# Kernel optimization log

Measured on AMD Instinct MI355X. Metric: run time of the kernel, lower is better.

Reference implementation:

```python
import jax, jax.numpy as jnp
import numpy as np

N, F_IN, F_OUT = 8192, 512, 128
NEG_SLOPE = 0.2
MASK_VAL = -9e16


def setup_inputs() -> dict:
    key = jax.random.key(0)
    k_x, k_adj, k_w, k_a = jax.random.split(key, 4)
    x = jax.random.normal(k_x, (N, F_IN), dtype=jnp.float32)
    adj = jax.random.randint(k_adj, (N, N), 0, 2, dtype=jnp.int32)
    # xavier_normal_ init: std = sqrt(2 / (fan_in + fan_out))
    w = jax.random.normal(k_w, (F_IN, F_OUT), dtype=jnp.float32) * np.sqrt(2.0 / (F_IN + F_OUT))
    a = jax.random.normal(k_a, (2 * F_OUT, 1), dtype=jnp.float32) * np.sqrt(2.0 / (2 * F_OUT + 1))
    return {"x": x, "adj": adj, "w": w, "a": a}


def reference(x, adj, w, a):
    f_out = w.shape[1]
    h = x @ w                                   # [N, f_out]
    source_scores = h @ a[:f_out]               # [N, 1]
    target_scores = h @ a[f_out:]               # [N, 1]
    e = source_scores + target_scores.T         # [N, N] outer sum
    e = jax.nn.leaky_relu(e, negative_slope=NEG_SLOPE)
    e = jnp.where(adj > 0, e, jnp.float32(MASK_VAL))
    attention = jax.nn.softmax(e, axis=-1)      # [N, N]
    h_prime = attention @ h                     # [N, f_out]
    return attention, h_prime
```

## Files before the change

kernel.cpp:

```cpp
#include <hip/hip_runtime.h>
#include <hip/hip_bf16.h>

typedef unsigned short u16;
typedef unsigned int u32;
typedef __attribute__((ext_vector_type(8))) short short8;
typedef __attribute__((ext_vector_type(4))) float f32x4;
typedef __attribute__((ext_vector_type(4))) int i32x4;

#define NN 8192
#define FIN 512
#define FOUT 128
#define NEG 0.2f
#define L2E 1.44269504088896340736f
#define EXP2(x) __builtin_amdgcn_exp2f(x)
#define LOG2(x) __builtin_amdgcn_logf(x)

__device__ __forceinline__ u16 f2bf(float f) {
  u32 u = __builtin_bit_cast(u32, f);
  u32 r = (u + 0x7fffu + ((u >> 16) & 1u)) >> 16;
  return (u16)r;
}

__global__ __launch_bounds__(256) void k_h(const float* __restrict__ x,
                                           const float* __restrict__ w,
                                           const float* __restrict__ av,
                                           u16* __restrict__ hb,
                                           float* __restrict__ sg,
                                           float* __restrict__ tgo) {
  __shared__ float xs[16][68];
  __shared__ float ws_[64][128];
  __shared__ u16 ht[16][130];
  const int t = threadIdx.x;
  const int r0 = blockIdx.x * 16;
  const int r = t >> 4;
  const int cq = (t & 15) * 4;
  float acc[2][4] = {};
  for (int kc = 0; kc < FIN; kc += 64) {
    __syncthreads();
    {
      const int rr = t >> 4, cc = (t & 15) * 4;
      *(float4*)&xs[rr][cc] = *(const float4*)(x + (size_t)(r0 + rr) * FIN + kc + cc);
    }
#pragma unroll
    for (int i = 0; i < 8; ++i) {
      const int off = i * 1024 + t * 4;
      const int wr = off >> 7, wc = off & 127;
      *(float4*)&ws_[wr][wc] = *(const float4*)(w + (size_t)(kc + wr) * FOUT + wc);
    }
    __syncthreads();
    for (int kk = 0; kk < 64; ++kk) {
      const float xv = xs[r][kk];
#pragma unroll
      for (int g = 0; g < 2; ++g) {
        const float4 wv = *(const float4*)&ws_[kk][cq + 64 * g];
        acc[g][0] = fmaf(xv, wv.x, acc[g][0]);
        acc[g][1] = fmaf(xv, wv.y, acc[g][1]);
        acc[g][2] = fmaf(xv, wv.z, acc[g][2]);
        acc[g][3] = fmaf(xv, wv.w, acc[g][3]);
      }
    }
  }
  const int rg = r0 + r;
  float sp = 0.f, tp = 0.f;
#pragma unroll
  for (int g = 0; g < 2; ++g) {
#pragma unroll
    for (int e = 0; e < 4; ++e) {
      const int n = cq + 64 * g + e;
      const float v = acc[g][e];
      ht[r][n] = f2bf(v);
      sp = fmaf(v, av[n], sp);
      tp = fmaf(v, av[FOUT + n], tp);
    }
  }
#pragma unroll
  for (int d = 1; d < 16; d <<= 1) {
    sp += __shfl_xor(sp, d);
    tp += __shfl_xor(tp, d);
  }
  if ((t & 15) == 0) { sg[rg] = sp; tgo[rg] = tp; }
  __syncthreads();
  {
    const int half = blockIdx.x & 1;
    u16* dst = hb + (size_t)(blockIdx.x >> 1) * 4096;
    union { short8 v; u16 us[8]; } b1;
    const int i1 = t * 8;
    const int o1 = (i1 >> 8) * 512 + half * 256 + (i1 & 255);
    const int nblk = i1 >> 8;
#pragma unroll
    for (int q = 0; q < 8; ++q) {
      const int j = (i1 + q) & 255;
      b1.us[q] = ht[((j >> 7) & 1) * 8 + (j & 7)][nblk * 16 + ((j >> 3) & 15)];
    }
    *(short8*)(dst + o1) = b1.v;
  }
}

__global__ __launch_bounds__(1024, 2) void k_maskA(const int* __restrict__ adj,
                                                   const float* __restrict__ sg,
                                                   const float* __restrict__ tg,
                                                   u32* __restrict__ maskR,
                                                   u32* __restrict__ maskT,
                                                   float* __restrict__ c2g) {
  __shared__ u32 mlds[32][257];
  const int tid = threadIdx.x;
  const int w = tid >> 6, lane = tid & 63;
  const int r0 = blockIdx.x << 5;
  const int rA = r0 + 2 * w, rB = rA + 1;
  const float sA = sg[rA], sB = sg[rB];
  const i32x4* apA = (const i32x4*)(adj + (size_t)rA * NN);
  const i32x4* apB = (const i32x4*)(adj + (size_t)rB * NN);
  float sumA = 0.f, sumB = 0.f;
#pragma unroll 2
  for (int it = 0; it < 32; ++it) {
    const i32x4 a0 = __builtin_nontemporal_load(apA + it * 64 + lane);
    const i32x4 a1 = __builtin_nontemporal_load(apB + it * 64 + lane);
    const float4 tv = *(const float4*)(tg + it * 256 + lane * 4);
    u32 nib0 = 0u, nib1 = 0u;
    {
      float e, p, sm = 0.f;
      e = sA + tv.x; e = fmaxf(e, NEG * e); p = EXP2(e * L2E); sm += (a0.x > 0) ? p : 0.f; nib0 |= (a0.x > 0) ? 1u : 0u;
      e = sA + tv.y; e = fmaxf(e, NEG * e); p = EXP2(e * L2E); sm += (a0.y > 0) ? p : 0.f; nib0 |= (a0.y > 0) ? 2u : 0u;
      e = sA + tv.z; e = fmaxf(e, NEG * e); p = EXP2(e * L2E); sm += (a0.z > 0) ? p : 0.f; nib0 |= (a0.z > 0) ? 4u : 0u;
      e = sA + tv.w; e = fmaxf(e, NEG * e); p = EXP2(e * L2E); sm += (a0.w > 0) ? p : 0.f; nib0 |= (a0.w > 0) ? 8u : 0u;
      sumA += sm;
    }
    {
      float e, p, sm = 0.f;
      e = sB + tv.x; e = fmaxf(e, NEG * e); p = EXP2(e * L2E); sm += (a1.x > 0) ? p : 0.f; nib1 |= (a1.x > 0) ? 1u : 0u;
      e = sB + tv.y; e = fmaxf(e, NEG * e); p = EXP2(e * L2E); sm += (a1.y > 0) ? p : 0.f; nib1 |= (a1.y > 0) ? 2u : 0u;
      e = sB + tv.z; e = fmaxf(e, NEG * e); p = EXP2(e * L2E); sm += (a1.z > 0) ? p : 0.f; nib1 |= (a1.z > 0) ? 4u : 0u;
      e = sB + tv.w; e = fmaxf(e, NEG * e); p = EXP2(e * L2E); sm += (a1.w > 0) ? p : 0.f; nib1 |= (a1.w > 0) ? 8u : 0u;
      sumB += sm;
    }
    u32 v0 = nib0;
    v0 |= __shfl_xor(v0, 1) << 4;
    v0 |= __shfl_xor(v0, 2) << 8;
    v0 |= __shfl_xor(v0, 4) << 16;
    u32 v1 = nib1;
    v1 |= __shfl_xor(v1, 1) << 4;
    v1 |= __shfl_xor(v1, 2) << 8;
    v1 |= __shfl_xor(v1, 4) << 16;
    if ((lane & 7) == 0) {
      mlds[2 * w][it * 8 + (lane >> 3)] = v0;
      mlds[2 * w + 1][it * 8 + (lane >> 3)] = v1;
    }
  }
#pragma unroll
  for (int d = 1; d < 64; d <<= 1) {
    sumA += __shfl_xor(sumA, d);
    sumB += __shfl_xor(sumB, d);
  }
  if (lane == 0) {
    c2g[rA] = -LOG2(sumA);
    c2g[rB] = -LOG2(sumB);
  }
  __syncthreads();
  for (int idx = tid; idx < 8192; idx += 1024) {
    const int wi = idx >> 5, rr = idx & 31;
    const u32 v = mlds[rr][wi];
    maskR[(size_t)(r0 + rr) * 256 + wi] = v;
    maskT[(size_t)wi * NN + r0 + rr] = v;
  }
}

__global__ __launch_bounds__(512, 4) void k_spv(const float* __restrict__ sg,
                                                const float* __restrict__ tg,
                                                const float* __restrict__ c2g,
                                                const u32* __restrict__ maskR,
                                                const u32* __restrict__ maskT,
                                                const u16* __restrict__ hb,
                                                float* __restrict__ att,
                                                float* __restrict__ part) {
  const int tid = threadIdx.x;
  const int w = tid >> 6, lane = tid & 63;
  if (blockIdx.x < 512) {
    const int mt = blockIdx.x >> 3, kt = blockIdx.x & 7;
    const int wr = w >> 1, ch = w & 1;
    const int wrow = mt * 128 + wr * 32;
    const int arow = lane & 15, kg = lane >> 4;
    const int rowA = wrow + arow, rowB = wrow + 16 + arow;
    const float sA = sg[rowA], cA = c2g[rowA];
    const float sB = sg[rowB], cB = c2g[rowB];
    f32x4 acc0[4], acc1[4];
#pragma unroll
    for (int j = 0; j < 4; ++j) {
      acc0[j] = (f32x4){0.f, 0.f, 0.f, 0.f};
      acc1[j] = (f32x4){0.f, 0.f, 0.f, 0.f};
    }
    const int kg8 = kg * 8;
#pragma unroll 2
    for (int step = 0; step < 32; ++step) {
      const int kgrp = kt * 32 + step;
      const int k0 = kgrp * 32;
      const u32 wdA = maskT[(size_t)kgrp * NN + rowA];
      const u32 wdB = maskT[(size_t)kgrp * NN + rowB];
      const u32 bA = (wdA >> kg8) & 0xffu;
      const u32 bB = (wdB >> kg8) & 0xffu;
      const float4 t0 = *(const float4*)(tg + k0 + kg8);
      const float4 t1 = *(const float4*)(tg + k0 + kg8 + 4);
      const float tv[8] = {t0.x, t0.y, t0.z, t0.w, t1.x, t1.y, t1.z, t1.w};
      union { short8 s8; u32 u[4]; } afA, afB;
      {
        float p[8];
#pragma unroll
        for (int e = 0; e < 8; ++e) {
          float ev = sA + tv[e];
          ev = fmaxf(ev, NEG * ev);
          p[e] = ((bA >> e) & 1u) ? EXP2(fmaf(ev, L2E, cA)) : 0.f;
        }
#pragma unroll
        for (int h2 = 0; h2 < 4; ++h2)
          afA.u[h2] = (u32)f2bf(p[2 * h2]) | ((u32)f2bf(p[2 * h2 + 1]) << 16);
      }
      {
        float p[8];
#pragma unroll
        for (int e = 0; e < 8; ++e) {
          float ev = sB + tv[e];
          ev = fmaxf(ev, NEG * ev);
          p[e] = ((bB >> e) & 1u) ? EXP2(fmaf(ev, L2E, cB)) : 0.f;
        }
#pragma unroll
        for (int h2 = 0; h2 < 4; ++h2)
          afB.u[h2] = (u32)f2bf(p[2 * h2]) | ((u32)f2bf(p[2 * h2 + 1]) << 16);
      }
      const u16* base = hb + (size_t)kgrp * 4096 + ch * 2048 + lane * 8;
#pragma unroll
      for (int j = 0; j < 4; ++j) {
        const short8 bf = *(const short8*)(base + j * 512);
        acc0[j] = __builtin_amdgcn_mfma_f32_16x16x32_bf16(afA.s8, bf, acc0[j], 0, 0, 0);
        acc1[j] = __builtin_amdgcn_mfma_f32_16x16x32_bf16(afB.s8, bf, acc1[j], 0, 0, 0);
      }
    }
    float* pslice = part + (size_t)kt * (NN * FOUT);
#pragma unroll
    for (int j = 0; j < 4; ++j) {
      const int col = (ch * 4 + j) * 16 + arow;
#pragma unroll
      for (int q = 0; q < 4; ++q) {
        pslice[(size_t)(wrow + kg * 4 + q) * FOUT + col] = acc0[j][q];
        pslice[(size_t)(wrow + 16 + kg * 4 + q) * FOUT + col] = acc1[j][q];
      }
    }
  } else {
    const int sb = blockIdx.x - 512;
    const int row = sb * 4 + (w >> 1);
    const int half = w & 1;
    const float sv = sg[row];
    const float c2 = c2g[row];
    const u32* mrow = maskR + (size_t)row * 256 + half * 128;
    const float* tbase = tg + half * 4096;
    float* abase = att + (size_t)row * NN + half * 4096;
    const u32 sh = (lane & 7) * 4;
#pragma unroll 4
    for (int it = 0; it < 16; ++it) {
      const int jo = it * 256 + lane * 4;
      const u32 wd = mrow[it * 8 + (lane >> 3)];
      const u32 nib = (wd >> sh) & 0xfu;
      const float4 tv = *(const float4*)(tbase + jo);
      float e0 = sv + tv.x; e0 = fmaxf(e0, NEG * e0);
      float e1 = sv + tv.y; e1 = fmaxf(e1, NEG * e1);
      float e2 = sv + tv.z; e2 = fmaxf(e2, NEG * e2);
      float e3 = sv + tv.w; e3 = fmaxf(e3, NEG * e3);
      f32x4 o;
      o.x = (nib & 1u) ? EXP2(fmaf(e0, L2E, c2)) : 0.f;
      o.y = (nib & 2u) ? EXP2(fmaf(e1, L2E, c2)) : 0.f;
      o.z = (nib & 4u) ? EXP2(fmaf(e2, L2E, c2)) : 0.f;
      o.w = (nib & 8u) ? EXP2(fmaf(e3, L2E, c2)) : 0.f;
      __builtin_nontemporal_store(o, (f32x4*)(abase + jo));
    }
  }
}

__global__ __launch_bounds__(256) void k_red(const float* __restrict__ part,
                                             float* __restrict__ hp) {
  const int i = (blockIdx.x * 256 + threadIdx.x) * 4;
  f32x4 s = (f32x4){0.f, 0.f, 0.f, 0.f};
#pragma unroll
  for (int kt = 0; kt < 8; ++kt)
    s += *(const f32x4*)(part + (size_t)kt * (NN * FOUT) + i);
  *(f32x4*)(hp + i) = s;
}

extern "C" void kernel_launch(void* const* d_in, const int* in_sizes, int n_in,
                              void* d_out, int out_size, void* d_ws, size_t ws_size,
                              hipStream_t stream) {
  const float* x = (const float*)d_in[0];
  const int* adj = (const int*)d_in[1];
  const float* w = (const float*)d_in[2];
  const float* a = (const float*)d_in[3];
  float* out = (float*)d_out;
  float* att = out;
  float* hp = out + (size_t)NN * NN;
  u16* hb = (u16*)d_ws;
  float* s = (float*)((char*)d_ws + (size_t)2 * 1024 * 1024);
  float* t = s + NN;
  float* c2 = t + NN;
  u32* maskR = (u32*)((char*)d_ws + (size_t)4 * 1024 * 1024);
  u32* maskT = (u32*)((char*)d_ws + (size_t)12 * 1024 * 1024);
  float* part = (float*)((char*)d_ws + (size_t)20 * 1024 * 1024);

  k_h<<<512, 256, 0, stream>>>(x, w, a, hb, s, t);
  k_maskA<<<256, 1024, 0, stream>>>(adj, s, t, maskR, maskT, c2);
  k_spv<<<2560, 512, 0, stream>>>(s, t, c2, maskR, maskT, hb, att, part);
  k_red<<<1024, 256, 0, stream>>>(part, hp);
}
```

Baseline: 173.0 us.

## Fuse attention write into mask kernel and split PV into its own kernel

The attention-matrix write moves into the mask/row-sum kernel, which reads mask bits straight from shared memory after computing each row's log-sum. This removes the row-major mask buffer and its write and read-back. The PV MFMA work becomes a standalone kernel with 512 blocks and a lower occupancy hint. The cost is that the 256MB attention store now runs in only 256 blocks and no longer overlaps with the MFMA work, as it did before inside the combined launch.

```diff
diff --git a/kernel.cpp b/kernel.cpp
--- a/kernel.cpp
+++ b/kernel.cpp
@@ -96,12 +96,12 @@
   }
 }
 
-__global__ __launch_bounds__(1024, 2) void k_maskA(const int* __restrict__ adj,
-                                                   const float* __restrict__ sg,
-                                                   const float* __restrict__ tg,
-                                                   u32* __restrict__ maskR,
-                                                   u32* __restrict__ maskT,
-                                                   float* __restrict__ c2g) {
+__global__ __launch_bounds__(1024, 2) void k_fms2(const int* __restrict__ adj,
+                                                  const float* __restrict__ sg,
+                                                  const float* __restrict__ tg,
+                                                  u32* __restrict__ maskT,
+                                                  float* __restrict__ c2g,
+                                                  float* __restrict__ att) {
   __shared__ u32 mlds[32][257];
   const int tid = threadIdx.x;
   const int w = tid >> 6, lane = tid & 63;
@@ -151,124 +151,123 @@
     sumA += __shfl_xor(sumA, d);
     sumB += __shfl_xor(sumB, d);
   }
+  const float c2A = -LOG2(sumA), c2B = -LOG2(sumB);
   if (lane == 0) {
-    c2g[rA] = -LOG2(sumA);
-    c2g[rB] = -LOG2(sumB);
+    c2g[rA] = c2A;
+    c2g[rB] = c2B;
   }
   __syncthreads();
   for (int idx = tid; idx < 8192; idx += 1024) {
     const int wi = idx >> 5, rr = idx & 31;
-    const u32 v = mlds[rr][wi];
-    maskR[(size_t)(r0 + rr) * 256 + wi] = v;
-    maskT[(size_t)wi * NN + r0 + rr] = v;
-  }
-}
-
-__global__ __launch_bounds__(512, 4) void k_spv(const float* __restrict__ sg,
-                                                const float* __restrict__ tg,
-                                                const float* __restrict__ c2g,
-                                                const u32* __restrict__ maskR,
-                                                const u32* __restrict__ maskT,
-                                                const u16* __restrict__ hb,
-                                                float* __restrict__ att,
-                                                float* __restrict__ part) {
+    maskT[(size_t)wi * NN + r0 + rr] = mlds[rr][wi];
+  }
+  float* aA = att + (size_t)rA * NN;
+  float* aB = att + (size_t)rB * NN;
+  const u32 sh = (lane & 7) * 4;
+#pragma unroll 2
+  for (int it = 0; it < 32; ++it) {
+    const int jo = it * 256 + lane * 4;
+    const float4 tv = *(const float4*)(tg + jo);
+    const int wi = it * 8 + (lane >> 3);
+    const u32 nibA = (mlds[2 * w][wi] >> sh) & 0xfu;
+    const u32 nibB = (mlds[2 * w + 1][wi] >> sh) & 0xfu;
+    float e0 = sA + tv.x; e0 = fmaxf(e0, NEG * e0);
+    float e1 = sA + tv.y; e1 = fmaxf(e1, NEG * e1);
+    float e2 = sA + tv.z; e2 = fmaxf(e2, NEG * e2);
+    float e3 = sA + tv.w; e3 = fmaxf(e3, NEG * e3);
+    f32x4 oA;
+    oA.x = (nibA & 1u) ? EXP2(fmaf(e0, L2E, c2A)) : 0.f;
+    oA.y = (nibA & 2u) ? EXP2(fmaf(e1, L2E, c2A)) : 0.f;
+    oA.z = (nibA & 4u) ? EXP2(fmaf(e2, L2E, c2A)) : 0.f;
+    oA.w = (nibA & 8u) ? EXP2(fmaf(e3, L2E, c2A)) : 0.f;
+    __builtin_nontemporal_store(oA, (f32x4*)(aA + jo));
+    e0 = sB + tv.x; e0 = fmaxf(e0, NEG * e0);
+    e1 = sB + tv.y; e1 = fmaxf(e1, NEG * e1);
+    e2 = sB + tv.z; e2 = fmaxf(e2, NEG * e2);
+    e3 = sB + tv.w; e3 = fmaxf(e3, NEG * e3);
+    f32x4 oB;
+    oB.x = (nibB & 1u) ? EXP2(fmaf(e0, L2E, c2B)) : 0.f;
+    oB.y = (nibB & 2u) ? EXP2(fmaf(e1, L2E, c2B)) : 0.f;
+    oB.z = (nibB & 4u) ? EXP2(fmaf(e2, L2E, c2B)) : 0.f;
+    oB.w = (nibB & 8u) ? EXP2(fmaf(e3, L2E, c2B)) : 0.f;
+    __builtin_nontemporal_store(oB, (f32x4*)(aB + jo));
+  }
+}
+
+__global__ __launch_bounds__(512, 2) void k_pv(const float* __restrict__ sg,
+                                               const float* __restrict__ tg,
+                                               const float* __restrict__ c2g,
+                                               const u32* __restrict__ maskT,
+                                               const u16* __restrict__ hb,
+                                               float* __restrict__ part) {
   const int tid = threadIdx.x;
   const int w = tid >> 6, lane = tid & 63;
-  if (blockIdx.x < 512) {
-    const int mt = blockIdx.x >> 3, kt = blockIdx.x & 7;
-    const int wr = w >> 1, ch = w & 1;
-    const int wrow = mt * 128 + wr * 32;
-    const int arow = lane & 15, kg = lane >> 4;
-    const int rowA = wrow + arow, rowB = wrow + 16 + arow;
-    const float sA = sg[rowA], cA = c2g[rowA];
-    const float sB = sg[rowB], cB = c2g[rowB];
-    f32x4 acc0[4], acc1[4];
+  const int mt = blockIdx.x >> 3, kt = blockIdx.x & 7;
+  const int wr = w >> 1, ch = w & 1;
+  const int wrow = mt * 128 + wr * 32;
+  const int arow = lane & 15, kg = lane >> 4;
+  const int rowA = wrow + arow, rowB = wrow + 16 + arow;
+  const float sA = sg[rowA], cA = c2g[rowA];
+  const float sB = sg[rowB], cB = c2g[rowB];
+  f32x4 acc0[4], acc1[4];
+#pragma unroll
+  for (int j = 0; j < 4; ++j) {
+    acc0[j] = (f32x4){0.f, 0.f, 0.f, 0.f};
+    acc1[j] = (f32x4){0.f, 0.f, 0.f, 0.f};
+  }
+  const int kg8 = kg * 8;
+#pragma unroll 2
+  for (int step = 0; step < 32; ++step) {
+    const int kgrp = kt * 32 + step;
+    const int k0 = kgrp * 32;
+    const u32 wdA = maskT[(size_t)kgrp * NN + rowA];
+    const u32 wdB = maskT[(size_t)kgrp * NN + rowB];
+    const u32 bA = (wdA >> kg8) & 0xffu;
+    const u32 bB = (wdB >> kg8) & 0xffu;
+    const float4 t0 = *(const float4*)(tg + k0 + kg8);
+    const float4 t1 = *(const float4*)(tg + k0 + kg8 + 4);
+    const float tv[8] = {t0.x, t0.y, t0.z, t0.w, t1.x, t1.y, t1.z, t1.w};
+    union { short8 s8; u32 u[4]; } afA, afB;
+    {
+      float p[8];
+#pragma unroll
+      for (int e = 0; e < 8; ++e) {
+        float ev = sA + tv[e];
+        ev = fmaxf(ev, NEG * ev);
+        p[e] = ((bA >> e) & 1u) ? EXP2(fmaf(ev, L2E, cA)) : 0.f;
+      }
+#pragma unroll
+      for (int h2 = 0; h2 < 4; ++h2)
+        afA.u[h2] = (u32)f2bf(p[2 * h2]) | ((u32)f2bf(p[2 * h2 + 1]) << 16);
+    }
+    {
+      float p[8];
+#pragma unroll
+      for (int e = 0; e < 8; ++e) {
+        float ev = sB + tv[e];
+        ev = fmaxf(ev, NEG * ev);
+        p[e] = ((bB >> e) & 1u) ? EXP2(fmaf(ev, L2E, cB)) : 0.f;
+      }
+#pragma unroll
+      for (int h2 = 0; h2 < 4; ++h2)
+        afB.u[h2] = (u32)f2bf(p[2 * h2]) | ((u32)f2bf(p[2 * h2 + 1]) << 16);
+    }
+    const u16* base = hb + (size_t)kgrp * 4096 + ch * 2048 + lane * 8;
 #pragma unroll
     for (int j = 0; j < 4; ++j) {
-      acc0[j] = (f32x4){0.f, 0.f, 0.f, 0.f};
-      acc1[j] = (f32x4){0.f, 0.f, 0.f, 0.f};
-    }
-    const int kg8 = kg * 8;
-#pragma unroll 2
-    for (int step = 0; step < 32; ++step) {
-      const int kgrp = kt * 32 + step;
-      const int k0 = kgrp * 32;
-      const u32 wdA = maskT[(size_t)kgrp * NN + rowA];
-      const u32 wdB = maskT[(size_t)kgrp * NN + rowB];
-      const u32 bA = (wdA >> kg8) & 0xffu;
-      const u32 bB = (wdB >> kg8) & 0xffu;
-      const float4 t0 = *(const float4*)(tg + k0 + kg8);
-      const float4 t1 = *(const float4*)(tg + k0 + kg8 + 4);
-      const float tv[8] = {t0.x, t0.y, t0.z, t0.w, t1.x, t1.y, t1.z, t1.w};
-      union { short8 s8; u32 u[4]; } afA, afB;
-      {
-        float p[8];
-#pragma unroll
-        for (int e = 0; e < 8; ++e) {
-          float ev = sA + tv[e];
-          ev = fmaxf(ev, NEG * ev);
-          p[e] = ((bA >> e) & 1u) ? EXP2(fmaf(ev, L2E, cA)) : 0.f;
-        }
-#pragma unroll
-        for (int h2 = 0; h2 < 4; ++h2)
-          afA.u[h2] = (u32)f2bf(p[2 * h2]) | ((u32)f2bf(p[2 * h2 + 1]) << 16);
-      }
-      {
-        float p[8];
-#pragma unroll
-        for (int e = 0; e < 8; ++e) {
-          float ev = sB + tv[e];
-          ev = fmaxf(ev, NEG * ev);
-          p[e] = ((bB >> e) & 1u) ? EXP2(fmaf(ev, L2E, cB)) : 0.f;
-        }
-#pragma unroll
-        for (int h2 = 0; h2 < 4; ++h2)
-          afB.u[h2] = (u32)f2bf(p[2 * h2]) | ((u32)f2bf(p[2 * h2 + 1]) << 16);
-      }
-      const u16* base = hb + (size_t)kgrp * 4096 + ch * 2048 + lane * 8;
-#pragma unroll
-      for (int j = 0; j < 4; ++j) {
-        const short8 bf = *(const short8*)(base + j * 512);
-        acc0[j] = __builtin_amdgcn_mfma_f32_16x16x32_bf16(afA.s8, bf, acc0[j], 0, 0, 0);
-        acc1[j] = __builtin_amdgcn_mfma_f32_16x16x32_bf16(afB.s8, bf, acc1[j], 0, 0, 0);
-      }
-    }
-    float* pslice = part + (size_t)kt * (NN * FOUT);
-#pragma unroll
-    for (int j = 0; j < 4; ++j) {
-      const int col = (ch * 4 + j) * 16 + arow;
-#pragma unroll
-      for (int q = 0; q < 4; ++q) {
-        pslice[(size_t)(wrow + kg * 4 + q) * FOUT + col] = acc0[j][q];
-        pslice[(size_t)(wrow + 16 + kg * 4 + q) * FOUT + col] = acc1[j][q];
-      }
-    }
-  } else {
-    const int sb = blockIdx.x - 512;
-    const int row = sb * 4 + (w >> 1);
-    const int half = w & 1;
-    const float sv = sg[row];
-    const float c2 = c2g[row];
-    const u32* mrow = maskR + (size_t)row * 256 + half * 128;
-    const float* tbase = tg + half * 4096;
-    float* abase = att + (size_t)row * NN + half * 4096;
-    const u32 sh = (lane & 7) * 4;
-#pragma unroll 4
-    for (int it = 0; it < 16; ++it) {
-      const int jo = it * 256 + lane * 4;
-      const u32 wd = mrow[it * 8 + (lane >> 3)];
-      const u32 nib = (wd >> sh) & 0xfu;
-      const float4 tv = *(const float4*)(tbase + jo);
-      float e0 = sv + tv.x; e0 = fmaxf(e0, NEG * e0);
-      float e1 = sv + tv.y; e1 = fmaxf(e1, NEG * e1);
-      float e2 = sv + tv.z; e2 = fmaxf(e2, NEG * e2);
-      float e3 = sv + tv.w; e3 = fmaxf(e3, NEG * e3);
-      f32x4 o;
-      o.x = (nib & 1u) ? EXP2(fmaf(e0, L2E, c2)) : 0.f;
-      o.y = (nib & 2u) ? EXP2(fmaf(e1, L2E, c2)) : 0.f;
-      o.z = (nib & 4u) ? EXP2(fmaf(e2, L2E, c2)) : 0.f;
-      o.w = (nib & 8u) ? EXP2(fmaf(e3, L2E, c2)) : 0.f;
-      __builtin_nontemporal_store(o, (f32x4*)(abase + jo));
+      const short8 bf = *(const short8*)(base + j * 512);
+      acc0[j] = __builtin_amdgcn_mfma_f32_16x16x32_bf16(afA.s8, bf, acc0[j], 0, 0, 0);
+      acc1[j] = __builtin_amdgcn_mfma_f32_16x16x32_bf16(afB.s8, bf, acc1[j], 0, 0, 0);
+    }
+  }
+  float* pslice = part + (size_t)kt * (NN * FOUT);
+#pragma unroll
+  for (int j = 0; j < 4; ++j) {
+    const int col = (ch * 4 + j) * 16 + arow;
+#pragma unroll
+    for (int q = 0; q < 4; ++q) {
+      pslice[(size_t)(wrow + kg * 4 + q) * FOUT + col] = acc0[j][q];
+      pslice[(size_t)(wrow + 16 + kg * 4 + q) * FOUT + col] = acc1[j][q];
     }
   }
 }
@@ -297,12 +296,11 @@
   float* s = (float*)((char*)d_ws + (size_t)2 * 1024 * 1024);
   float* t = s + NN;
   float* c2 = t + NN;
-  u32* maskR = (u32*)((char*)d_ws + (size_t)4 * 1024 * 1024);
-  u32* maskT = (u32*)((char*)d_ws + (size_t)12 * 1024 * 1024);
-  float* part = (float*)((char*)d_ws + (size_t)20 * 1024 * 1024);
+  u32* maskT = (u32*)((char*)d_ws + (size_t)4 * 1024 * 1024);
+  float* part = (float*)((char*)d_ws + (size_t)12 * 1024 * 1024);
 
   k_h<<<512, 256, 0, stream>>>(x, w, a, hb, s, t);
-  k_maskA<<<256, 1024, 0, stream>>>(adj, s, t, maskR, maskT, c2);
-  k_spv<<<2560, 512, 0, stream>>>(s, t, c2, maskR, maskT, hb, att, part);
+  k_fms2<<<256, 1024, 0, stream>>>(adj, s, t, maskT, c2, att);
+  k_pv<<<512, 512, 0, stream>>>(s, t, c2, maskT, hb, part);
   k_red<<<1024, 256, 0, stream>>>(part, hp);
 }
```

After: 189.8 us. 9.7% more time.
